# Optimization experiments

Hardware: AMD Instinct MI355X
Metric: run time of the kernel (lower is better)

The kernel has to match this reference:

```python
import jax, jax.numpy as jnp
import numpy as np
from jax import lax

EPS = 1e-12  # torch F.normalize eps
DN = ('NCHW', 'OIHW', 'NCHW')


def setup_inputs() -> dict:
    B, C, H, W, K = 16, 64, 192, 192, 3
    key = jax.random.key(0)
    k1, k2, k3 = jax.random.split(key, 3)
    x = jax.random.normal(k1, (B, C, H, W), dtype=jnp.float32)
    # Conv2d(n_feat, 2*n_feat, 3, stride=3, bias=False) weight
    w_qk = jax.random.normal(k2, (2 * C, C, 3, 3), dtype=jnp.float32) * np.float32(np.sqrt(1.0 / (C * 9)))
    # Parameter(C,C,K,K), kaiming_normal_ (fan_in=C*K*K, gain=sqrt(2)) then *0.1
    std = np.float32(np.sqrt(2.0 / (C * K * K)) * 0.1)
    weight = jax.random.normal(k3, (C, C, K, K), dtype=jnp.float32) * std
    # temperature Parameter (1,1,1); init zeros in the module, use 0.5 so the
    # dynamic-kernel branch is exercised numerically
    temperature = jnp.full((1, 1, 1), 0.5, dtype=jnp.float32)
    return {"x": x, "w_qk": w_qk, "weight": weight, "temperature": temperature}


def _l2_normalize_per_sample(t):
    # t: (B, ...) -> L2-normalize flattened per sample (torch F.normalize)
    n = jnp.sqrt(jnp.sum(t.reshape(t.shape[0], -1) ** 2, axis=-1))
    n = jnp.maximum(n, EPS).reshape((t.shape[0],) + (1,) * (t.ndim - 1))
    return t / n


def reference(x, w_qk, weight, temperature):
    B, C, H, W = x.shape
    K = weight.shape[-1]
    S = 2 * K - 1  # 5: number of spatial shifts in the cross-covariance
    P = K - 1

    # qk conv: stride-3 valid conv -> (B, 2C, H2, W2)
    qk = lax.conv_general_dilated(x, w_qk, (3, 3), 'VALID', dimension_numbers=DN)
    q, k = jnp.split(qk, 2, axis=1)
    q = _l2_normalize_per_sample(q)
    k = _l2_normalize_per_sample(k)
    H2, W2 = q.shape[2], q.shape[3]

    # cal_xtx: attn[b, co, ci, i, j] = sum_{h,w} q_pad[b, ci, i+h, j+w] * k[b, co, h, w]
    q_pad = jnp.pad(q, ((0, 0), (0, 0), (P, P), (P, P)))
    rows = []
    for i in range(S):  # fixed small 5x5 shift set
        row = []
        for j in range(S):
            sl = lax.dynamic_slice(q_pad, (0, 0, i, j), (B, C, H2, W2))
            row.append(jnp.einsum('bchw,bdhw->bdc', sl, k))  # (B, co, ci)
        rows.append(jnp.stack(row, axis=-1))
    attn = jnp.stack(rows, axis=-2)  # (B, C, C, S, S)

    # conv2d(attn.view(B*C, C, S, S), weight) valid -> (B*C, C, K, K)
    ak = lax.conv_general_dilated(attn.reshape(B * C, C, S, S), weight, (1, 1), 'VALID', dimension_numbers=DN)
    ak = ak.reshape(B, C, C, K, K).transpose(0, 2, 1, 3, 4)  # swap the two C dims

    # normalize each (C,K,K) slice per (b, c0)
    n = jnp.sqrt(jnp.sum(ak.reshape(B, C, -1) ** 2, axis=-1))
    ak = ak / jnp.maximum(n, EPS)[:, :, None, None, None]

    kern = weight[None] + ak * temperature  # (B, C, C, K, K)

    # sample-wise conv2d: groups=B trick
    out = lax.conv_general_dilated(
        x.reshape(1, B * C, H, W), kern.reshape(B * C, C, K, K), (1, 1),
        [(K // 2, K // 2)] * 2, dimension_numbers=DN, feature_group_count=B)
    return jax.nn.relu(out.reshape(B, C, H, W))
```

## Files before the change

kernel.cpp:

```cpp
#include <hip/hip_runtime.h>
#include <cstddef>

#define BB 16
#define CC_ 64
#define HH 192
#define WW 192
#define HW2 4096
#define XPH 194
#define XPW 196

typedef _Float16 f16x8 __attribute__((ext_vector_type(8)));
typedef float f32x4 __attribute__((ext_vector_type(4)));

__global__ __launch_bounds__(1024) void k_wpack(const float* __restrict__ wqk,
                                                _Float16* __restrict__ wh) {
  int e = blockIdx.x * 1024 + threadIdx.x;
  int co = e / 576, t = e % 576;
  int ci = t / 9, rs = t % 9;
  int r = rs / 3, s = rs % 3;
  int ch = ci >> 5, t32 = ci & 31;
  wh[(((r * 2 + ch) * 128 + co) * 96) + s * 32 + t32] = (_Float16)wqk[e];
}

__global__ __launch_bounds__(256) void k_xhalo(_Float16* __restrict__ xh) {
  int e = blockIdx.x * 256 + threadIdx.x;
  int b = e / 9280, i = e % 9280;
  int r, px, c;
  if (i < 3136) {
    r = (i < 1568) ? 0 : 193;
    int j = (i < 1568) ? i : i - 1568;
    px = j >> 3;
    c = j & 7;
  } else {
    int i2 = i - 3136;
    r = 1 + (i2 >> 5);
    int rem = i2 & 31;
    int sel = rem >> 3;
    px = (sel == 0) ? 0 : 192 + sel;
    c = rem & 7;
  }
  *(f16x8*)(xh + (((size_t)b * XPH + r) * XPW + px) * 64 + c * 8) =
      (f16x8)(_Float16)0;
}

__global__ __launch_bounds__(256) void k_xpack(const float* __restrict__ x,
                                               _Float16* __restrict__ xh) {
  int blk = blockIdx.x;
  int xg = blk % 3;
  int t = blk / 3;
  int y = t % 192, b = t / 192;
  int x0 = xg * 64;
  __shared__ _Float16 tl[64 * 72];
  int tid = threadIdx.x;
  int ci = tid >> 2, c4 = (tid & 3) * 16;
  const float* xp = x + ((size_t)(b * 64 + ci) * HH + y) * WW + x0 + c4;
#pragma unroll
  for (int i = 0; i < 4; ++i) {
    float4 v = *(const float4*)(xp + i * 4);
    tl[(c4 + i * 4 + 0) * 72 + ci] = (_Float16)v.x;
    tl[(c4 + i * 4 + 1) * 72 + ci] = (_Float16)v.y;
    tl[(c4 + i * 4 + 2) * 72 + ci] = (_Float16)v.z;
    tl[(c4 + i * 4 + 3) * 72 + ci] = (_Float16)v.w;
  }
  __syncthreads();
#pragma unroll
  for (int i = 0; i < 2; ++i) {
    int e = tid + 256 * i;
    int col = e >> 3, g = e & 7;
    *(f16x8*)(xh + (((size_t)b * XPH + y + 1) * XPW + x0 + 1 + col) * 64 + g * 8) =
        *(f16x8*)&tl[col * 72 + g * 8];
  }
}

__global__ __launch_bounds__(256) void k_qkconv(const _Float16* __restrict__ xh,
                                                const _Float16* __restrict__ wh,
                                                _Float16* __restrict__ qkh) {
  int blk = blockIdx.x;
  int pt = blk & 31, b = blk >> 5;
  int tid = threadIdx.x;
  int w = tid >> 6, lane = tid & 63, n16 = lane & 15, quad = lane >> 4;
  int mh = w & 1, nh = w >> 1;
  const _Float16* xb = xh + (size_t)b * (XPH * XPW * 64);

  f32x4 acc[4][4];
#pragma unroll
  for (int mt = 0; mt < 4; ++mt)
#pragma unroll
    for (int nt = 0; nt < 4; ++nt) acc[mt][nt] = (f32x4){0.f, 0.f, 0.f, 0.f};

#pragma unroll
  for (int kc = 0; kc < 6; ++kc) {
    int r = kc >> 1, ch = kc & 1;
    int irow = 6 * pt + 3 * nh + r;
    const _Float16* wp = wh + (size_t)kc * (128 * 96);
#pragma unroll
    for (int s = 0; s < 3; ++s) {
      f16x8 af[4], bf[4];
#pragma unroll
      for (int mt = 0; mt < 4; ++mt)
        af[mt] = *(const f16x8*)(wp + (mh * 64 + mt * 16 + n16) * 96 + s * 32 +
                                 quad * 8);
#pragma unroll
      for (int nt = 0; nt < 4; ++nt) {
        int col = 3 * (nt * 16 + n16) + s;
        bf[nt] = *(const f16x8*)(xb + ((size_t)(irow + 1) * XPW + col + 1) * 64 +
                                 ch * 32 + quad * 8);
      }
#pragma unroll
      for (int mt = 0; mt < 4; ++mt)
#pragma unroll
        for (int nt = 0; nt < 4; ++nt)
          acc[mt][nt] = __builtin_amdgcn_mfma_f32_16x16x32_f16(af[mt], bf[nt],
                                                               acc[mt][nt], 0, 0, 0);
    }
  }
  int py = pt * 2 + nh;
#pragma unroll
  for (int mt = 0; mt < 4; ++mt)
#pragma unroll
    for (int reg = 0; reg < 4; ++reg) {
      int co = mh * 64 + mt * 16 + quad * 4 + reg;
      _Float16* op = qkh + (size_t)(b * 128 + co) * HW2 + py * 64;
#pragma unroll
      for (int nt = 0; nt < 4; ++nt) op[nt * 16 + n16] = (_Float16)acc[mt][nt][reg];
    }
}

__global__ __launch_bounds__(256) void k_qpad(const _Float16* __restrict__ qkh,
                                              _Float16* __restrict__ qpad) {
  int blk = blockIdx.x;
  int b = blk >> 6, ci = blk & 63;
  __shared__ _Float16 qrow[4096];
  int tid = threadIdx.x;
  const _Float16* src = qkh + (size_t)(b * 128 + ci) * HW2;
#pragma unroll
  for (int i = 0; i < 2; ++i)
    ((f16x8*)qrow)[tid + 256 * i] = ((const f16x8*)src)[tid + 256 * i];
  __syncthreads();
  _Float16* dst = qpad + ((size_t)(b * 5) * 64 + ci) * 4352;
  const f16x8 zero = (f16x8)(_Float16)0;
  for (int it = tid; it < 544; it += 256) {
    int w8 = it & 7, hr = it >> 3;
    int h = hr - 2;
    bool rowok = (unsigned)h < 64u;
    f16x8 vm = (rowok && w8 > 0) ? *(const f16x8*)&qrow[h * 64 + w8 * 8 - 8] : zero;
    f16x8 vc = rowok ? *(const f16x8*)&qrow[h * 64 + w8 * 8] : zero;
    f16x8 vp = (rowok && w8 < 7) ? *(const f16x8*)&qrow[h * 64 + w8 * 8 + 8] : zero;
#pragma unroll
    for (int djx = 0; djx < 5; ++djx) {
      const int s = djx - 2;
      f16x8 r;
#pragma unroll
      for (int j = 0; j < 8; ++j) {
        const int rel = j + s;
        r[j] = (rel < 0) ? vm[8 + rel] : ((rel < 8) ? vc[rel] : vp[rel - 8]);
      }
      *(f16x8*)(dst + (size_t)djx * (64 * 4352) + hr * 64 + w8 * 8) = r;
    }
  }
}

__global__ __launch_bounds__(512) void k_attn(const _Float16* __restrict__ qkh,
                                              const _Float16* __restrict__ qpad,
                                              float* __restrict__ attn_p) {
  int blk = blockIdx.x;
  int xcd = blk & 7, j = blk >> 3;
  int b = xcd + ((j >= 25) ? 8 : 0);
  int sh = (j >= 25) ? (j - 25) : j;
  int djx = sh % 5, dix = sh / 5;
  int tid = threadIdx.x, w = tid >> 6, lane = tid & 63;
  int n16 = lane & 15, quad = lane >> 4;
  int g = w >> 1, h = w & 1;

  __shared__ float lpart[4096];

  const _Float16* ka = qkh + (size_t)(b * 128 + 64 + g * 16 + n16) * HW2 +
                       h * 2048 + quad * 8;
  const _Float16* qa = qpad + ((size_t)(b * 5 + djx) * 64 + n16) * 4352 +
                       dix * 64 + h * 2048 + quad * 8;

  f32x4 acc[4];
#pragma unroll
  for (int nt = 0; nt < 4; ++nt) acc[nt] = (f32x4){0.f, 0.f, 0.f, 0.f};

  f16x8 afS[4], bfS[4][4];
#define LDSLOT(sl, k_)                                                         \
  {                                                                            \
    afS[sl] = *(const f16x8*)(ka + (k_)*32);                                   \
    _Pragma("unroll") for (int nt = 0; nt < 4; ++nt) bfS[sl][nt] =             \
        *(const f16x8*)(qa + (size_t)nt * 69632 + (k_)*32);                    \
  }
  LDSLOT(0, 0) LDSLOT(1, 1) LDSLOT(2, 2) LDSLOT(3, 3)

#pragma unroll
  for (int ks = 0; ks < 64; ++ks) {
    const int sl = ks & 3;
#pragma unroll
    for (int nt = 0; nt < 4; ++nt)
      acc[nt] = __builtin_amdgcn_mfma_f32_16x16x32_f16(afS[sl], bfS[sl][nt],
                                                       acc[nt], 0, 0, 0);
    if (ks + 4 < 64) LDSLOT(sl, ks + 4)
  }
#undef LDSLOT

  if (h == 0) {
#pragma unroll
    for (int nt = 0; nt < 4; ++nt)
#pragma unroll
      for (int reg = 0; reg < 4; ++reg)
        lpart[(g * 16 + quad * 4 + reg) * 64 + nt * 16 + n16] = acc[nt][reg];
  }
  __syncthreads();
  if (h == 1) {
    float* op = attn_p + (size_t)(b * 25 + sh) * 4096;
#pragma unroll
    for (int nt = 0; nt < 4; ++nt)
#pragma unroll
      for (int reg = 0; reg < 4; ++reg) {
        int idx = (g * 16 + quad * 4 + reg) * 64 + nt * 16 + n16;
        op[idx] = lpart[idx] + acc[nt][reg];
      }
  }
}

__global__ __launch_bounds__(576) void k_akconv(const float* __restrict__ attn_p,
                                                const float* __restrict__ wgt,
                                                float* __restrict__ akt) {
  int blk = blockIdx.x;
  int b = blk >> 6, co = blk & 63;
  __shared__ float sa[64 * 25];
  int tid = threadIdx.x;
  for (int e = tid; e < 1600; e += 576) {
    int didj = e >> 6, ci = e & 63;
    size_t idx = (((size_t)b * 25 + didj) * 64 + co) * 64 + ci;
    sa[ci * 25 + didj] = attn_p[idx];
  }
  __syncthreads();
  int o = tid / 9, rs = tid % 9;
  int ki = rs / 3, kj = rs % 3;
  float acc = 0.f;
  for (int ci = 0; ci < 64; ++ci) {
    const float* wp = wgt + (o * 64 + ci) * 9;
    const float* ap = sa + ci * 25 + ki * 5 + kj;
#pragma unroll
    for (int r = 0; r < 3; ++r)
#pragma unroll
      for (int s = 0; s < 3; ++s) acc += ap[r * 5 + s] * wp[r * 3 + s];
  }
  akt[((size_t)(b * 64 + o) * 64 + co) * 9 + rs] = acc;
}

__global__ __launch_bounds__(576) void k_kern(const float* __restrict__ akt,
                                              const float* __restrict__ wgt,
                                              const float* __restrict__ temp,
                                              _Float16* __restrict__ kh) {
  int blk = blockIdx.x;
  int o = blk & 63;
  int tid = threadIdx.x;
  float v = akt[(size_t)blk * 576 + tid];
  float sq = v * v;
#pragma unroll
  for (int m = 1; m < 64; m <<= 1) sq += __shfl_xor(sq, m, 64);
  __shared__ float wsum[9];
  if ((tid & 63) == 0) wsum[tid >> 6] = sq;
  __syncthreads();
  float tot = 0.f;
#pragma unroll
  for (int i = 0; i < 9; ++i) tot += wsum[i];
  float inv = temp[0] / fmaxf(sqrtf(tot), 1e-12f);
  float kv = wgt[o * 576 + tid] + v * inv;
  int b = blk >> 6;
  int ci = tid / 9, rs = tid % 9;
  kh[(((size_t)(b * 9 + rs) * 64 + o) * 64) + ci] = (_Float16)kv;
}

__global__ __launch_bounds__(256, 3) void k_final(const _Float16* __restrict__ xh,
                                                  const _Float16* __restrict__ kh,
                                                  float* __restrict__ out) {
  int blk = blockIdx.x;
  int xt = blk % 3;
  int t2 = blk / 3;
  int yt = t2 % 48, b = t2 / 48;
  int y0 = yt * 4, x0 = xt * 64;

  __shared__ __align__(16) _Float16 xs[6 * 68 * 64];

  int tid = threadIdx.x;
  int w = tid >> 6, lane = tid & 63;
  int n16 = lane & 15, quad = lane >> 4;

  const _Float16* xb = xh + (size_t)b * (XPH * XPW * 64);
  const _Float16* kb = kh + (size_t)b * (9 * 64 * 64);

  {
    f16x8 v[13];
#pragma unroll
    for (int i = 0; i < 13; ++i) {
      int e = tid + 256 * i;
      if (e < 3264) {
        int row = e / 544, rem = e % 544;
        int px = rem >> 3, c = rem & 7;
        v[i] = *(const f16x8*)(xb + ((size_t)(y0 + row) * XPW + x0 + px) * 64 +
                               c * 8);
      }
    }
#pragma unroll
    for (int i = 0; i < 13; ++i) {
      int e = tid + 256 * i;
      if (e < 3264) {
        int row = e / 544, rem = e % 544;
        int px = rem >> 3, c = rem & 7;
        *(f16x8*)&xs[((row * 68 + px) * 8 + (c ^ (px & 7))) * 8] = v[i];
      }
    }
  }
  __syncthreads();

  f32x4 acc[4][4];
#pragma unroll
  for (int mt = 0; mt < 4; ++mt)
#pragma unroll
    for (int nt = 0; nt < 4; ++nt) acc[mt][nt] = (f32x4){0.f, 0.f, 0.f, 0.f};

#define LDAF(dst, ch_)                                                          \
  {                                                                             \
    const int rs_ = (ch_) >> 1, hi_ = (ch_)&1;                                  \
    _Pragma("unroll") for (int mt = 0; mt < 4; ++mt) dst[mt] =                  \
        *(const f16x8*)(kb + ((size_t)rs_ * 64 + mt * 16 + n16) * 64 +          \
                        hi_ * 32 + quad * 8);                                   \
  }

  f16x8 af[3][4];
  LDAF(af[0], 0)
  LDAF(af[1], 1)

#pragma unroll
  for (int ch = 0; ch < 18; ++ch) {
    if (ch + 2 < 18) LDAF(af[(ch + 2) % 3], ch + 2)
    int rs = ch >> 1, hi = ch & 1;
    int r = rs / 3, s = rs % 3;
    int trow = w + r;
    f16x8 bf[4];
#pragma unroll
    for (int nt = 0; nt < 4; ++nt) {
      int px = nt * 16 + n16 + s;
      int c = (hi * 4 + quad) ^ (px & 7);
      bf[nt] = *(const f16x8*)&xs[((trow * 68 + px) * 8 + c) * 8];
    }
#pragma unroll
    for (int mt = 0; mt < 4; ++mt)
#pragma unroll
      for (int nt = 0; nt < 4; ++nt)
        acc[mt][nt] = __builtin_amdgcn_mfma_f32_16x16x32_f16(af[ch % 3][mt],
                                                             bf[nt], acc[mt][nt],
                                                             0, 0, 0);
  }
#undef LDAF

  int y = y0 + w;
#pragma unroll
  for (int mt = 0; mt < 4; ++mt)
#pragma unroll
    for (int reg = 0; reg < 4; ++reg) {
      int o = mt * 16 + quad * 4 + reg;
      float* op = out + (((size_t)(b * 64 + o) * HH + y) * WW + x0);
#pragma unroll
      for (int nt = 0; nt < 4; ++nt)
        op[nt * 16 + n16] = fmaxf(acc[mt][nt][reg], 0.f);
    }
}

extern "C" void kernel_launch(void* const* d_in, const int* in_sizes, int n_in,
                              void* d_out, int out_size, void* d_ws, size_t ws_size,
                              hipStream_t stream) {
  const float* x = (const float*)d_in[0];
  const float* wqk = (const float*)d_in[1];
  const float* wgt = (const float*)d_in[2];
  const float* temp = (const float*)d_in[3];
  float* out = (float*)d_out;
  char* ws = (char*)d_ws;

  _Float16* xh = (_Float16*)ws;
  _Float16* qkh = (_Float16*)(ws + 77873152);
  _Float16* qpad = (_Float16*)(ws + 94650368);
  float* attn_p = (float*)(ws + 139214848);
  _Float16* wh = (_Float16*)(ws + 139067392);
  float* akt = (float*)(ws + 94650368);
  _Float16* kh = (_Float16*)(ws + 97009664);

  k_wpack<<<dim3(72), 1024, 0, stream>>>(wqk, wh);
  k_xhalo<<<dim3(580), 256, 0, stream>>>(xh);
  k_xpack<<<dim3(9216), 256, 0, stream>>>(x, xh);
  k_qkconv<<<dim3(512), 256, 0, stream>>>(xh, wh, qkh);
  k_qpad<<<dim3(1024), 256, 0, stream>>>(qkh, qpad);
  k_attn<<<dim3(400), 512, 0, stream>>>(qkh, qpad, attn_p);
  k_akconv<<<dim3(1024), 576, 0, stream>>>(attn_p, wgt, akt);
  k_kern<<<dim3(1024), 576, 0, stream>>>(akt, wgt, temp, kh);
  k_final<<<dim3(2304), 256, 0, stream>>>(xh, kh, out);
}
```

Before: 598.8 us.

## Restructure attn kernel to reuse K fragments across five row shifts

The qk conv now writes the k half of its output in an MFMA-fragment-friendly tiled layout via LDS, so the attention kernel can load it with coalesced per-lane vectors. The attention kernel drops from 400 to 80 blocks. Each block handles one column shift, streams padded q rows through double-buffered, XOR-swizzled LDS, and keeps a register ring of k fragments so that all five row shifts reuse the same loads. This cuts redundant global reads of q and k and removes the LDS partial-sum reduction. In exchange, the grid now fills far fewer CUs and register pressure rises (ring of 13 plus 10 accumulators).

```diff
diff --git a/kernel.cpp b/kernel.cpp
--- a/kernel.cpp
+++ b/kernel.cpp
@@ -82,6 +82,8 @@
   int mh = w & 1, nh = w >> 1;
   const _Float16* xb = xh + (size_t)b * (XPH * XPW * 64);
 
+  __shared__ _Float16 lds_k[16 * 64 * 8];
+
   f32x4 acc[4][4];
 #pragma unroll
   for (int mt = 0; mt < 4; ++mt)
@@ -115,15 +117,39 @@
     }
   }
   int py = pt * 2 + nh;
-#pragma unroll
-  for (int mt = 0; mt < 4; ++mt)
-#pragma unroll
-    for (int reg = 0; reg < 4; ++reg) {
-      int co = mh * 64 + mt * 16 + quad * 4 + reg;
-      _Float16* op = qkh + (size_t)(b * 128 + co) * HW2 + py * 64;
-#pragma unroll
-      for (int nt = 0; nt < 4; ++nt) op[nt * 16 + n16] = (_Float16)acc[mt][nt][reg];
-    }
+  if (mh == 0) {
+#pragma unroll
+    for (int mt = 0; mt < 4; ++mt)
+#pragma unroll
+      for (int reg = 0; reg < 4; ++reg) {
+        int co = mt * 16 + quad * 4 + reg;
+        _Float16* op = qkh + (size_t)(b * 128 + co) * HW2 + py * 64;
+#pragma unroll
+        for (int nt = 0; nt < 4; ++nt) op[nt * 16 + n16] = (_Float16)acc[mt][nt][reg];
+      }
+  } else {
+#pragma unroll
+    for (int mt = 0; mt < 4; ++mt)
+#pragma unroll
+      for (int nt = 0; nt < 4; ++nt)
+#pragma unroll
+        for (int reg = 0; reg < 4; ++reg) {
+          int plocal = nh * 64 + nt * 16 + n16;
+          int tile = mt * 4 + (plocal >> 5);
+          int lanep = ((plocal >> 3) & 3) * 16 + quad * 4 + reg;
+          lds_k[(tile * 64 + lanep) * 8 + (plocal & 7)] = (_Float16)acc[mt][nt][reg];
+        }
+  }
+  __syncthreads();
+  _Float16* ka2b = qkh + (size_t)(b * 128 + 64) * HW2;
+#pragma unroll
+  for (int r = 0; r < 4; ++r) {
+    int e = tid + 256 * r;
+    int tile = e >> 6, lanep = e & 63;
+    int g = tile >> 2, sp = pt * 4 + (tile & 3);
+    *(f16x8*)(ka2b + ((size_t)(g * 128 + sp) * 64 + lanep) * 8) =
+        *(f16x8*)&lds_k[e * 8];
+  }
 }
 
 __global__ __launch_bounds__(256) void k_qpad(const _Float16* __restrict__ qkh,
@@ -165,61 +191,79 @@
                                               float* __restrict__ attn_p) {
   int blk = blockIdx.x;
   int xcd = blk & 7, j = blk >> 3;
-  int b = xcd + ((j >= 25) ? 8 : 0);
-  int sh = (j >= 25) ? (j - 25) : j;
-  int djx = sh % 5, dix = sh / 5;
+  int b = xcd + ((j >= 5) ? 8 : 0);
+  int djx = (j >= 5) ? (j - 5) : j;
   int tid = threadIdx.x, w = tid >> 6, lane = tid & 63;
   int n16 = lane & 15, quad = lane >> 4;
-  int g = w >> 1, h = w & 1;
-
-  __shared__ float lpart[4096];
-
-  const _Float16* ka = qkh + (size_t)(b * 128 + 64 + g * 16 + n16) * HW2 +
-                       h * 2048 + quad * 8;
-  const _Float16* qa = qpad + ((size_t)(b * 5 + djx) * 64 + n16) * 4352 +
-                       dix * 64 + h * 2048 + quad * 8;
-
-  f32x4 acc[4];
-#pragma unroll
-  for (int nt = 0; nt < 4; ++nt) acc[nt] = (f32x4){0.f, 0.f, 0.f, 0.f};
-
-  f16x8 afS[4], bfS[4][4];
-#define LDSLOT(sl, k_)                                                         \
-  {                                                                            \
-    afS[sl] = *(const f16x8*)(ka + (k_)*32);                                   \
-    _Pragma("unroll") for (int nt = 0; nt < 4; ++nt) bfS[sl][nt] =             \
-        *(const f16x8*)(qa + (size_t)nt * 69632 + (k_)*32);                    \
-  }
-  LDSLOT(0, 0) LDSLOT(1, 1) LDSLOT(2, 2) LDSLOT(3, 3)
-
-#pragma unroll
-  for (int ks = 0; ks < 64; ++ks) {
-    const int sl = ks & 3;
-#pragma unroll
-    for (int nt = 0; nt < 4; ++nt)
-      acc[nt] = __builtin_amdgcn_mfma_f32_16x16x32_f16(afS[sl], bfS[sl][nt],
-                                                       acc[nt], 0, 0, 0);
-    if (ks + 4 < 64) LDSLOT(sl, ks + 4)
-  }
-#undef LDSLOT
-
-  if (h == 0) {
-#pragma unroll
-    for (int nt = 0; nt < 4; ++nt)
+  int g = w & 3, cih = w >> 2;
+
+  __shared__ __align__(16) _Float16 qs[2][64 * 128];
+
+  const _Float16* kaw = qkh + (size_t)(b * 128 + 64) * HW2 + (size_t)g * 65536 +
+                        lane * 8;
+  const _Float16* qpb = qpad + (size_t)((b * 5 + djx) * 64) * 4352;
+
+  int srow = tid >> 3, sch = (tid & 7) * 2;
+  const _Float16* qsrc = qpb + (size_t)srow * 4352 + sch * 8;
+  int so0 = srow * 128 + ((sch ^ (srow & 15)) * 8);
+  int so1 = srow * 128 + (((sch + 1) ^ (srow & 15)) * 8);
+
+  f32x4 acc[5][2];
+#pragma unroll
+  for (int d = 0; d < 5; ++d)
+#pragma unroll
+    for (int nt = 0; nt < 2; ++nt) acc[d][nt] = (f32x4){0.f, 0.f, 0.f, 0.f};
+
+  f16x8 ring[13];
+#pragma unroll
+  for (int p = 0; p < 4; ++p) ring[p] = *(const f16x8*)(kaw + p * 512);
+
+  f16x8 sA = *(const f16x8*)(qsrc);
+  f16x8 sB = *(const f16x8*)(qsrc + 8);
+  *(f16x8*)&qs[0][so0] = sA;
+  *(f16x8*)&qs[0][so1] = sB;
+  __syncthreads();
+
+#pragma unroll
+  for (int c = 0; c < 34; ++c) {
+    if (c < 33) {
+      sA = *(const f16x8*)(qsrc + (c + 1) * 128);
+      sB = *(const f16x8*)(qsrc + (c + 1) * 128 + 8);
+    }
+#pragma unroll
+    for (int ss = 0; ss < 4; ++ss) {
+      const int S = c * 4 + ss;
+      if (S + 4 <= 127)
+        ring[(S + 4) % 13] = *(const f16x8*)(kaw + (S + 4) * 512);
+      const _Float16* qb = qs[c & 1];
+      const int chs = ((ss * 4 + quad) ^ n16) * 8;
+      f16x8 bf0 = *(const f16x8*)&qb[(cih * 32 + n16) * 128 + chs];
+      f16x8 bf1 = *(const f16x8*)&qb[(cih * 32 + 16 + n16) * 128 + chs];
+#pragma unroll
+      for (int d = 0; d < 5; ++d)
+        if (S >= 2 * d && S <= 2 * d + 127) {
+          acc[d][0] = __builtin_amdgcn_mfma_f32_16x16x32_f16(
+              ring[(S - 2 * d) % 13], bf0, acc[d][0], 0, 0, 0);
+          acc[d][1] = __builtin_amdgcn_mfma_f32_16x16x32_f16(
+              ring[(S - 2 * d) % 13], bf1, acc[d][1], 0, 0, 0);
+        }
+    }
+    if (c < 33) {
+      *(f16x8*)&qs[(c + 1) & 1][so0] = sA;
+      *(f16x8*)&qs[(c + 1) & 1][so1] = sB;
+      __syncthreads();
+    }
+  }
+
+#pragma unroll
+  for (int d = 0; d < 5; ++d) {
+    float* op = attn_p + (size_t)(b * 25 + d * 5 + djx) * 4096;
+#pragma unroll
+    for (int nt = 0; nt < 2; ++nt)
 #pragma unroll
       for (int reg = 0; reg < 4; ++reg)
-        lpart[(g * 16 + quad * 4 + reg) * 64 + nt * 16 + n16] = acc[nt][reg];
-  }
-  __syncthreads();
-  if (h == 1) {
-    float* op = attn_p + (size_t)(b * 25 + sh) * 4096;
-#pragma unroll
-    for (int nt = 0; nt < 4; ++nt)
-#pragma unroll
-      for (int reg = 0; reg < 4; ++reg) {
-        int idx = (g * 16 + quad * 4 + reg) * 64 + nt * 16 + n16;
-        op[idx] = lpart[idx] + acc[nt][reg];
-      }
+        op[(g * 16 + quad * 4 + reg) * 64 + cih * 32 + nt * 16 + n16] =
+            acc[d][nt][reg];
   }
 }
 
@@ -393,7 +437,7 @@
   k_xpack<<<dim3(9216), 256, 0, stream>>>(x, xh);
   k_qkconv<<<dim3(512), 256, 0, stream>>>(xh, wh, qkh);
   k_qpad<<<dim3(1024), 256, 0, stream>>>(qkh, qpad);
-  k_attn<<<dim3(400), 512, 0, stream>>>(qkh, qpad, attn_p);
+  k_attn<<<dim3(80), 512, 0, stream>>>(qkh, qpad, attn_p);
   k_akconv<<<dim3(1024), 576, 0, stream>>>(attn_p, wgt, akt);
   k_kern<<<dim3(1024), 576, 0, stream>>>(akt, wgt, temp, kh);
   k_final<<<dim3(2304), 256, 0, stream>>>(xh, kh, out);
```

After: 493.0 us. -17.7%, faster.
